# Optimization experiments

Measured on AMD Instinct MI355X. Metric: run time of the kernel, lower is better.

## Reference

```python
import jax, jax.numpy as jnp
import numpy as np

H = 8            # kv heads
R = 2            # qhead_ratio -> hq = 16 query heads
D = 128          # head_size
DEG = 2          # power degree
GATE_OFFSET = 6.906768  # ~log(999), gates start near 1


def setup_inputs() -> dict:
    key = jax.random.key(0)
    ks = jax.random.split(key, 7)
    B, T, C = 1, 2048, 2048
    q_dim = H * R * D   # 2048
    kv_dim = H * D      # 1024
    s = 0.02
    return {
        "hidden_states": jax.random.normal(ks[0], (B, T, C), dtype=jnp.float32),
        "Wq": jax.random.normal(ks[1], (C, q_dim), dtype=jnp.float32) * s,
        "Wk": jax.random.normal(ks[2], (C, kv_dim), dtype=jnp.float32) * s,
        "Wv": jax.random.normal(ks[3], (C, kv_dim), dtype=jnp.float32) * s,
        "Wg": jax.random.normal(ks[4], (C, H), dtype=jnp.float32) * s,
        "Wc": jax.random.normal(ks[5], (q_dim, C), dtype=jnp.float32) * s,
        "bc": jnp.zeros((C,), dtype=jnp.float32),
    }


def _power_attention(q, k, v, log_g):
    # q: [B,T,hq,D], k/v: [B,T,H,D], log_g: [B,T,H]
    B, T, hq, d = q.shape
    scale = 1.0 / d ** 0.5
    # GQA: query head i uses kv head i // R (q was viewed as (B,T,H,R,D))
    k = jnp.repeat(k, R, axis=2)            # [B,T,hq,D]
    v = jnp.repeat(v, R, axis=2)            # [B,T,hq,D]
    logG = jnp.cumsum(log_g, axis=1)        # [B,T,H]
    logG = jnp.repeat(logG, R, axis=2)      # [B,T,hq]
    logG = jnp.transpose(logG, (0, 2, 1))   # [B,hq,T]
    qk = jnp.einsum('bthd,bshd->bhts', q, k) * scale   # [B,hq,T,T]
    a = qk ** DEG                                       # even degree -> >= 0
    # gating decay exp(logG_t - logG_s) <= 1 for s <= t
    gate = logG[:, :, :, None] - logG[:, :, None, :]    # [B,hq,T,T]
    causal = jnp.tril(jnp.ones((T, T), dtype=bool))
    a = jnp.where(causal, a * jnp.exp(gate), 0.0)
    norm = jnp.sum(a, axis=-1) + 1e-6                   # [B,hq,T]
    y = jnp.einsum('bhts,bshd->bthd', a, v)             # [B,T,hq,D]
    y = y / jnp.transpose(norm, (0, 2, 1))[..., None]
    return y


def reference(hidden_states, Wq, Wk, Wv, Wg, Wc, bc):
    B, T, C = hidden_states.shape
    q = (hidden_states @ Wq).reshape(B, T, H * R, D)
    k = (hidden_states @ Wk).reshape(B, T, H, D)
    v = (hidden_states @ Wv).reshape(B, T, H, D)
    g = hidden_states @ Wg                              # [B,T,H]
    log_g = jax.nn.log_sigmoid(GATE_OFFSET + g.astype(jnp.float32))
    y = _power_attention(q, k, v, log_g)                # [B,T,hq,D]
    y = y.reshape(B, T, H * R * D)
    return y @ Wc + bc
```

## Files before the change

### kernel.cpp

```cpp
#include <hip/hip_runtime.h>

typedef unsigned short u16;
typedef unsigned int u32;
typedef unsigned long long u64;
typedef __bf16 bf16x8 __attribute__((ext_vector_type(8)));
typedef float f32x4 __attribute__((ext_vector_type(4)));

union FragAB {
  bf16x8 v;
  u16 u[8];
  u32 w[4];
  u64 d2[2];
};

__device__ __forceinline__ u16 f2bf(float f) {
  u32 u = __builtin_bit_cast(u32, f);
  u += 0x7fffu + ((u >> 16) & 1u);
  return (u16)(u >> 16);
}

__device__ __forceinline__ void gload_lds16(const void* g, void* l) {
  __builtin_amdgcn_global_load_lds((__attribute__((address_space(1))) void*)g,
                                   (__attribute__((address_space(3))) void*)l, 16, 0, 0);
}

__device__ __forceinline__ int permcol(int n) {
  int k = n & 31;
  return (n & ~31) | ((k & 12) << 1) | ((k & 16) >> 2) | (k & 3);
}

__global__ __launch_bounds__(256) void conv_bf16_kernel(const float* __restrict__ in,
                                                        u16* __restrict__ out, int n4) {
  int i = blockIdx.x * 256 + threadIdx.x;
  if (i >= n4) return;
  float4 v = ((const float4*)in)[i];
  u32 lo = (u32)f2bf(v.x) | ((u32)f2bf(v.y) << 16);
  u32 hi = (u32)f2bf(v.z) | ((u32)f2bf(v.w) << 16);
  ((u32*)out)[2 * i] = lo;
  ((u32*)out)[2 * i + 1] = hi;
}

__global__ __launch_bounds__(256) void tconv_kernel(const float* __restrict__ in,
                                                    u16* __restrict__ out, int K, int N) {
  __shared__ float tile[32][33];
  int col = threadIdx.x & 31;
  int row0 = threadIdx.x >> 5;
  int kb = blockIdx.y * 32, nb = blockIdx.x * 32;
#pragma unroll
  for (int i = 0; i < 4; i++) {
    int r = row0 + i * 8;
    tile[r][col] = in[(size_t)(kb + r) * N + nb + col];
  }
  __syncthreads();
#pragma unroll
  for (int i = 0; i < 4; i++) {
    int r = row0 + i * 8;
    out[(size_t)(nb + r) * K + kb + col] = f2bf(tile[col][r]);
  }
}

__global__ __launch_bounds__(256) void tconv3_kernel(const float* __restrict__ Wq,
                                                     const float* __restrict__ Wk,
                                                     const float* __restrict__ Wv,
                                                     u16* __restrict__ slab) {
  __shared__ float tile[32][33];
  const int z = blockIdx.z;
  const float* src = (z < 2) ? Wq : (z == 2 ? Wk : Wv);
  const int srcN = (z < 2) ? 2048 : 1024;
  const int colBase = (z == 1) ? 1024 : 0;
  const int dstRowBase = z * 1024;
  int col = threadIdx.x & 31;
  int row0 = threadIdx.x >> 5;
  int kb = blockIdx.y * 32, nb = blockIdx.x * 32;
#pragma unroll
  for (int i = 0; i < 4; i++) {
    int r = row0 + i * 8;
    tile[r][col] = src[(size_t)(kb + r) * srcN + colBase + nb + col];
  }
  __syncthreads();
#pragma unroll
  for (int i = 0; i < 4; i++) {
    int r = row0 + i * 8;
    slab[(size_t)(dstRowBase + nb + r) * 2048 + kb + col] = f2bf(tile[col][r]);
  }
}

__global__ __launch_bounds__(256) void gate_kernel(const float* __restrict__ hs,
                                                   const float* __restrict__ Wg,
                                                   float* __restrict__ lgt) {
  int lane = threadIdx.x & 63, wid = threadIdx.x >> 6;
  int t = blockIdx.x * 4 + wid;
  float acc[8] = {0.f, 0.f, 0.f, 0.f, 0.f, 0.f, 0.f, 0.f};
  for (int c = lane; c < 2048; c += 64) {
    float x = hs[(size_t)t * 2048 + c];
    float4 w0 = *(const float4*)&Wg[c * 8];
    float4 w1 = *(const float4*)&Wg[c * 8 + 4];
    acc[0] += x * w0.x; acc[1] += x * w0.y; acc[2] += x * w0.z; acc[3] += x * w0.w;
    acc[4] += x * w1.x; acc[5] += x * w1.y; acc[6] += x * w1.z; acc[7] += x * w1.w;
  }
#pragma unroll
  for (int h = 0; h < 8; h++) {
    float v = acc[h];
    for (int m = 1; m < 64; m <<= 1) v += __shfl_xor(v, m, 64);
    if (lane == 0) {
      float x = 6.906768f + v;
      lgt[h * 2048 + t] = -log1pf(__expf(-x));
    }
  }
}

__global__ __launch_bounds__(256) void cumsum_kernel(const float* __restrict__ lgt,
                                                     float* __restrict__ logG) {
  int h = blockIdx.x;
  __shared__ float buf[2048];
  for (int i = threadIdx.x; i < 2048; i += 256) buf[i] = lgt[h * 2048 + i];
  __syncthreads();
  for (int off = 1; off < 2048; off <<= 1) {
    float tmp[8];
#pragma unroll
    for (int j = 0; j < 8; j++) {
      int i = threadIdx.x + j * 256;
      tmp[j] = (i >= off) ? buf[i - off] : 0.f;
    }
    __syncthreads();
#pragma unroll
    for (int j = 0; j < 8; j++) {
      int i = threadIdx.x + j * 256;
      buf[i] += tmp[j];
    }
    __syncthreads();
  }
  for (int i = threadIdx.x; i < 2048; i += 256) logG[h * 2048 + i] = buf[i];
}

template <int MODE, int NT>
__global__ __launch_bounds__(512) void gemm_bf16(const u16* __restrict__ A,
                                                 const u16* __restrict__ BT,
                                                 void* __restrict__ C0,
                                                 void* __restrict__ C1,
                                                 int permLim) {
  __shared__ __align__(16) u16 As[128 * 64];
  __shared__ __align__(16) u16 Bs[128 * 64];
  constexpr int nwg = 16 * NT * (MODE == 2 ? 2 : 1);
  constexpr int cpx = nwg >> 3;
  const int raw = (int)blockIdx.x;
  const int wg = (raw & 7) * cpx + (raw >> 3);
  int bx, by, z;
  if constexpr (MODE == 2) {
    z = wg & 1;
    int t = wg >> 1;
    by = t >> 4;
    bx = t & 15;
  } else {
    z = 0;
    by = wg >> 4;
    bx = wg & 15;
  }
  const int kBeg = (MODE == 2) ? z * 1024 : 0;
  const int kEnd = (MODE == 2) ? kBeg + 1024 : 2048;
  constexpr int N = NT * 128;

  const int tid = threadIdx.x;
  const int lane = tid & 63, wid = tid >> 6;
  const int m0 = bx * 128, n0 = by * 128;
  const int wr = wid >> 2, wc = wid & 3;
  const int l15 = lane & 15, kg = lane >> 4;

  f32x4 acc[4][2];
#pragma unroll
  for (int i = 0; i < 4; i++)
#pragma unroll
    for (int j = 0; j < 2; j++) acc[i][j] = f32x4{0.f, 0.f, 0.f, 0.f};

  const int ch0 = (wid * 2) * 64 + lane;
  const int ch1 = ch0 + 64;
  const int r0 = ch0 >> 3, u0 = (ch0 & 7) ^ (r0 & 7);
  const int r1 = ch1 >> 3, u1 = (ch1 & 7) ^ (r1 & 7);
  const u16* Asrc0 = A + (size_t)(m0 + r0) * 2048 + u0 * 8;
  const u16* Asrc1 = A + (size_t)(m0 + r1) * 2048 + u1 * 8;
  const u16* Bsrc0 = BT + (size_t)(n0 + r0) * 2048 + u0 * 8;
  const u16* Bsrc1 = BT + (size_t)(n0 + r1) * 2048 + u1 * 8;
  u16* Adst0 = As + (wid * 2) * 512;
  u16* Bdst0 = Bs + (wid * 2) * 512;

  for (int k0 = kBeg; k0 < kEnd; k0 += 64) {
    __syncthreads();
    gload_lds16(Asrc0 + k0, Adst0);
    gload_lds16(Asrc1 + k0, Adst0 + 512);
    gload_lds16(Bsrc0 + k0, Bdst0);
    gload_lds16(Bsrc1 + k0, Bdst0 + 512);
    __syncthreads();

#pragma unroll
    for (int ks = 0; ks < 2; ks++) {
      FragAB af[4], bfr[2];
      const int ul = ks * 4 + (kg >> 1);
#pragma unroll
      for (int mt = 0; mt < 4; mt++) {
        int row = wr * 64 + mt * 16 + l15;
        int sw = row & 7;
        const u16* p = &As[row * 64 + (kg & 1) * 4];
        af[mt].d2[0] = *(const u64*)&p[(ul ^ sw) << 3];
        af[mt].d2[1] = *(const u64*)&p[((ul + 2) ^ sw) << 3];
      }
#pragma unroll
      for (int nt = 0; nt < 2; nt++) {
        int row = wc * 32 + nt * 16 + l15;
        int sw = row & 7;
        const u16* p = &Bs[row * 64 + (kg & 1) * 4];
        bfr[nt].d2[0] = *(const u64*)&p[(ul ^ sw) << 3];
        bfr[nt].d2[1] = *(const u64*)&p[((ul + 2) ^ sw) << 3];
      }
#pragma unroll
      for (int mt = 0; mt < 4; mt++)
#pragma unroll
        for (int nt = 0; nt < 2; nt++)
          acc[mt][nt] = __builtin_amdgcn_mfma_f32_16x16x32_bf16(af[mt].v, bfr[nt].v, acc[mt][nt], 0, 0, 0);
    }
  }

#pragma unroll
  for (int mt = 0; mt < 4; mt++) {
#pragma unroll
    for (int re = 0; re < 4; re++) {
      int m = m0 + wr * 64 + mt * 16 + kg * 4 + re;
#pragma unroll
      for (int nt = 0; nt < 2; nt++) {
        int n = n0 + wc * 32 + nt * 16 + l15;
        float v = acc[mt][nt][re];
        if constexpr (MODE == 2) {
          float* P = z ? (float*)C1 : (float*)C0;
          P[(size_t)m * N + n] = v;
        } else {
          int nw = (n < permLim) ? permcol(n) : n;
          ((u16*)C0)[(size_t)m * N + nw] = f2bf(v);
        }
      }
    }
  }
}

__global__ __launch_bounds__(256, 2) void power_attn(const u16* __restrict__ QKV,
                                                     const float* __restrict__ logG,
                                                     float* __restrict__ y0p,
                                                     float* __restrict__ y1p,
                                                     float* __restrict__ npart) {
  __shared__ __align__(16) u16 Ks[2 * 64 * 128];
  __shared__ __align__(16) u16 Vt[2 * 128 * 64];
  __shared__ float eS[2 * 64];

  const int raw = (int)blockIdx.x;
  const int orig = (raw & 7) * 64 + (raw >> 3);
  const int hq = orig >> 5;
  const int j_ = orig & 31;
  const int half = j_ & 1;
  const int bslot = j_ >> 1;
  const int qa = (bslot + (hq >> 1) * 3) & 15;
  const int qt = (hq & 1) ? (15 - qa) : qa;
  const int hk = hq >> 1;
  const int t0 = qt * 128;

  const int tid = threadIdx.x, lane = tid & 63, wid = tid >> 6;
  const int l15 = lane & 15, kg = lane >> 4;
  const int l7 = l15 & 7;

  const int s4 = tid & 15, dgrp = tid >> 4;
  const int ubase = 4 * (s4 >> 3) + (s4 & 3);
  const int vhb = (s4 >> 2) & 1;

  const u16* Kbase = QKV + 2048 + hk * 128;
  const u16* Vbase = QKV + 3072 + hk * 128 + dgrp * 8;
  const float* lgh = logG + hk * 2048;

  FragAB qf[2][4];
  float celg[2];
  int myT[2];
  const float scale2 = 0.0078125f;
#pragma unroll
  for (int cg = 0; cg < 2; cg++) {
    myT[cg] = t0 + wid * 16 + cg * 64 + l15;
    const u16* qrow = QKV + (size_t)myT[cg] * 4096 + hq * 128;
#pragma unroll
    for (int ks = 0; ks < 4; ks++) qf[cg][ks].v = *(const bf16x8*)(qrow + ks * 32 + kg * 8);
    celg[cg] = scale2 * __expf(lgh[myT[cg]]);
  }

  f32x4 yacc[8][2];
#pragma unroll
  for (int i = 0; i < 8; i++)
#pragma unroll
    for (int c = 0; c < 2; c++) yacc[i][c] = f32x4{0.f, 0.f, 0.f, 0.f};
  float nacc[2] = {0.f, 0.f};

  const int itBeg = half ? (qt + 1) : 0;
  const int itEnd = half ? (2 * qt + 2) : (qt + 1);

  auto stageK = [&](int s0, int bb) {
#pragma unroll
    for (int c = 0; c < 4; c++) {
      int ch = (wid * 4 + c) * 64 + lane;
      int row = ch >> 4, du = ch & 15;
      int su = du ^ (row & 7);
      gload_lds16(Kbase + (size_t)(s0 + row) * 4096 + su * 8, &Ks[bb * 8192 + (wid * 4 + c) * 512]);
    }
  };
  auto loadV = [&](int s0, uint4* vr) {
#pragma unroll
    for (int r = 0; r < 4; r++) vr[r] = *(const uint4*)(Vbase + (size_t)(s0 + 4 * s4 + r) * 4096);
  };
  auto writeV = [&](int bb, const uint4* vr) {
    u16* vd = &Vt[bb * 8192];
    const u32* w0 = (const u32*)&vr[0];
    const u32* w1 = (const u32*)&vr[1];
    const u32* w2 = (const u32*)&vr[2];
    const u32* w3 = (const u32*)&vr[3];
#pragma unroll
    for (int i = 0; i < 8; i++) {
      u32 sel = (i & 1) ? 0x07060302u : 0x05040100u;
      u32 lo = __builtin_amdgcn_perm(w1[i >> 1], w0[i >> 1], sel);
      u32 hi = __builtin_amdgcn_perm(w3[i >> 1], w2[i >> 1], sel);
      int d = dgrp * 8 + i;
      int e = d * 64 + 8 * (ubase ^ i) + 4 * vhb;
      *(u64*)&vd[e] = (u64)lo | ((u64)hi << 32);
    }
  };

  {
    uint4 vr[4];
    stageK(itBeg * 64, 0);
    loadV(itBeg * 64, vr);
    float ee = (tid < 64) ? lgh[itBeg * 64 + tid] : 0.f;
    writeV(0, vr);
    if (tid < 64) eS[tid] = __expf(-ee);
  }
  __syncthreads();

  for (int it = itBeg; it < itEnd; it++) {
    const int cur = (it - itBeg) & 1;
    const int s0 = it * 64;
    const bool hasNext = (it + 1 < itEnd);
    uint4 vr[4];
    float ee = 0.f;
    if (hasNext) {
      stageK(s0 + 64, cur ^ 1);
      loadV(s0 + 64, vr);
      if (tid < 64) ee = lgh[s0 + 64 + tid];
    }

    const u16* kb = &Ks[cur * 8192];
    f32x4 sacc[4][2];
#pragma unroll
    for (int mt = 0; mt < 4; mt++)
#pragma unroll
      for (int cg = 0; cg < 2; cg++) sacc[mt][cg] = f32x4{0.f, 0.f, 0.f, 0.f};
    __builtin_amdgcn_s_setprio(1);
#pragma unroll
    for (int ks = 0; ks < 4; ks++) {
#pragma unroll
      for (int mt = 0; mt < 4; mt++) {
        FragAB af;
        af.v = *(const bf16x8*)&kb[(mt * 16 + l15) * 128 + 8 * ((4 * ks + kg) ^ l7)];
        sacc[mt][0] = __builtin_amdgcn_mfma_f32_16x16x32_bf16(af.v, qf[0][ks].v, sacc[mt][0], 0, 0, 0);
        sacc[mt][1] = __builtin_amdgcn_mfma_f32_16x16x32_bf16(af.v, qf[1][ks].v, sacc[mt][1], 0, 0, 0);
      }
    }
    __builtin_amdgcn_s_setprio(0);

    FragAB pa[2][2];
    const bool need_mask = (it >= 2 * qt);
#pragma unroll
    for (int mt = 0; mt < 4; mt++) {
      f32x4 ev = *(const f32x4*)&eS[cur * 64 + mt * 16 + kg * 4];
#pragma unroll
      for (int cg = 0; cg < 2; cg++) {
        u32 pb[4];
#pragma unroll
        for (int r = 0; r < 4; r++) {
          float x = sacc[mt][cg][r];
          float p = x * x * celg[cg] * ev[r];
          if (need_mask) {
            int s = s0 + mt * 16 + kg * 4 + r;
            p = (s <= myT[cg]) ? p : 0.f;
          }
          nacc[cg] += p;
          pb[r] = __builtin_bit_cast(u32, p) + 0x8000u;
        }
        pa[cg][mt >> 1].w[(mt & 1) * 2 + 0] = __builtin_amdgcn_perm(pb[1], pb[0], 0x07060302u);
        pa[cg][mt >> 1].w[(mt & 1) * 2 + 1] = __builtin_amdgcn_perm(pb[3], pb[2], 0x07060302u);
      }
    }

    const u16* vb = &Vt[cur * 8192];
    const int x0 = 8 * (kg ^ l7);
    __builtin_amdgcn_s_setprio(1);
#pragma unroll
    for (int ksv = 0; ksv < 2; ksv++) {
      const int xo = x0 ^ (ksv * 32);
#pragma unroll
      for (int nt = 0; nt < 8; nt++) {
        FragAB bfv;
        bfv.v = *(const bf16x8*)&vb[(nt * 16 + l15) * 64 + xo];
        yacc[nt][0] = __builtin_amdgcn_mfma_f32_16x16x32_bf16(pa[0][ksv].v, bfv.v, yacc[nt][0], 0, 0, 0);
        yacc[nt][1] = __builtin_amdgcn_mfma_f32_16x16x32_bf16(pa[1][ksv].v, bfv.v, yacc[nt][1], 0, 0, 0);
      }
    }
    __builtin_amdgcn_s_setprio(0);

    if (hasNext) {
      writeV(cur ^ 1, vr);
      if (tid < 64) eS[(cur ^ 1) * 64 + tid] = __expf(-ee);
    }
    __syncthreads();
  }

  float* yp = half ? y1p : y0p;
  float* np = npart + half * (16 * 2048);
#pragma unroll
  for (int cg = 0; cg < 2; cg++) {
    float nf = nacc[cg];
    nf += __shfl_xor(nf, 16, 64);
    nf += __shfl_xor(nf, 32, 64);
    if (lane < 16) np[hq * 2048 + t0 + wid * 16 + cg * 64 + lane] = nf;
#pragma unroll
    for (int re = 0; re < 4; re++) {
      int trow = t0 + wid * 16 + cg * 64 + kg * 4 + re;
      float* yrow = yp + (size_t)trow * 2048 + hq * 128;
#pragma unroll
      for (int nt = 0; nt < 8; nt++) yrow[nt * 16 + l15] = yacc[nt][cg][re];
    }
  }
}

__global__ __launch_bounds__(256) void combine_kernel(const float* __restrict__ y0,
                                                      const float* __restrict__ y1,
                                                      const float* __restrict__ npart,
                                                      u16* __restrict__ yb) {
  int i = blockIdx.x * 256 + threadIdx.x;
  int e0 = i << 2;
  int t = e0 >> 11;
  int hq = (e0 >> 7) & 15;
  float nn = npart[hq * 2048 + t] + npart[32768 + hq * 2048 + t] + 1e-6f;
  float inv = 1.0f / nn;
  float4 a = ((const float4*)y0)[i];
  float4 b = ((const float4*)y1)[i];
  u32 lo = (u32)f2bf((a.x + b.x) * inv) | ((u32)f2bf((a.y + b.y) * inv) << 16);
  u32 hi = (u32)f2bf((a.z + b.z) * inv) | ((u32)f2bf((a.w + b.w) * inv) << 16);
  ((u32*)yb)[2 * i] = lo;
  ((u32*)yb)[2 * i + 1] = hi;
}

__global__ __launch_bounds__(256) void combine2_kernel(const float* __restrict__ p0,
                                                       float* __restrict__ out,
                                                       const float* __restrict__ bias) {
  int i = blockIdx.x * 256 + threadIdx.x;
  int col = (i << 2) & 2047;
  float4 a = ((const float4*)p0)[i];
  float4 b = ((const float4*)out)[i];
  float4 bb = *(const float4*)&bias[col];
  float4 r;
  r.x = a.x + b.x + bb.x;
  r.y = a.y + b.y + bb.y;
  r.z = a.z + b.z + bb.z;
  r.w = a.w + b.w + bb.w;
  ((float4*)out)[i] = r;
}

extern "C" void kernel_launch(void* const* d_in, const int* in_sizes, int n_in,
                              void* d_out, int out_size, void* d_ws, size_t ws_size,
                              hipStream_t stream) {
  (void)in_sizes; (void)n_in; (void)out_size; (void)ws_size;
  const float* hs = (const float*)d_in[0];
  const float* Wq = (const float*)d_in[1];
  const float* Wk = (const float*)d_in[2];
  const float* Wv = (const float*)d_in[3];
  const float* Wg = (const float*)d_in[4];
  const float* Wc = (const float*)d_in[5];
  const float* bc = (const float*)d_in[6];
  float* out = (float*)d_out;

  char* ws = (char*)d_ws;
  const size_t MB = 1024 * 1024;
  u16* slab   = (u16*)(ws);
  u16* hs_bf  = (u16*)(ws + 16 * MB);
  u16* qkv_bf = (u16*)(ws + 24 * MB);
  float* y0p  = (float*)(ws + 40 * MB);
  float* npart = (float*)(ws + 56 * MB);
  float* lgt  = (float*)(ws + 56 * MB + 262144);
  float* logG = (float*)(ws + 56 * MB + 327680);
  float* y1p = out;
  u16* y_bf = hs_bf;
  u16* WcT = slab;

  conv_bf16_kernel<<<4096, 256, 0, stream>>>(hs, hs_bf, 2048 * 2048 / 4);
  tconv3_kernel<<<dim3(32, 64, 4), 256, 0, stream>>>(Wq, Wk, Wv, slab);

  gemm_bf16<1, 32><<<512, 512, 0, stream>>>(hs_bf, slab, qkv_bf, nullptr, 3072);

  gate_kernel<<<512, 256, 0, stream>>>(hs, Wg, lgt);
  cumsum_kernel<<<8, 256, 0, stream>>>(lgt, logG);

  tconv_kernel<<<dim3(64, 64), 256, 0, stream>>>(Wc, WcT, 2048, 2048);

  power_attn<<<dim3(512), 256, 0, stream>>>(qkv_bf, logG, y0p, y1p, npart);
  combine_kernel<<<4096, 256, 0, stream>>>(y0p, y1p, npart, y_bf);

  gemm_bf16<2, 16><<<512, 512, 0, stream>>>(y_bf, WcT, y0p, out, 0);
  combine2_kernel<<<4096, 256, 0, stream>>>(y0p, out, bc);
}
```

Before: 199.2 us.

## Double-buffer GEMM LDS tiles and pre-permute K columns for single 128-bit fragment loads

The GEMM now uses two LDS buffers and issues the global-to-LDS loads for the next K tile before computing the current one. This removes one barrier per iteration and lets memory latency overlap with MFMA work. The producers (hs conversion, weight transposes, combine) now write K columns in a permuted order, so each lane can read its MFMA fragment with one 16-byte LDS load instead of two 8-byte loads. The cost is double the LDS footprint, which may lower occupancy, and correctness depends on both GEMM operands using the same K permutation.

```diff
diff --git a/kernel.cpp b/kernel.cpp
--- a/kernel.cpp
+++ b/kernel.cpp
@@ -29,15 +29,18 @@
   return (n & ~31) | ((k & 12) << 1) | ((k & 16) >> 2) | (k & 3);
 }
 
-__global__ __launch_bounds__(256) void conv_bf16_kernel(const float* __restrict__ in,
+__global__ __launch_bounds__(256) void conv_perm_kernel(const float* __restrict__ in,
                                                         u16* __restrict__ out, int n4) {
   int i = blockIdx.x * 256 + threadIdx.x;
   if (i >= n4) return;
   float4 v = ((const float4*)in)[i];
-  u32 lo = (u32)f2bf(v.x) | ((u32)f2bf(v.y) << 16);
-  u32 hi = (u32)f2bf(v.z) | ((u32)f2bf(v.w) << 16);
-  ((u32*)out)[2 * i] = lo;
-  ((u32*)out)[2 * i + 1] = hi;
+  u64 pk = (u64)f2bf(v.x) | ((u64)f2bf(v.y) << 16) | ((u64)f2bf(v.z) << 32) |
+           ((u64)f2bf(v.w) << 48);
+  int col = (i << 2) & 2047;
+  int g = (col >> 2) & 7;
+  int ncol = (col & ~31) | ((2 * (g & 3) + (g >> 2)) << 2);
+  size_t row = (size_t)(i >> 9);
+  *(u64*)&out[row * 2048 + ncol] = pk;
 }
 
 __global__ __launch_bounds__(256) void tconv_kernel(const float* __restrict__ in,
@@ -46,6 +49,7 @@
   int col = threadIdx.x & 31;
   int row0 = threadIdx.x >> 5;
   int kb = blockIdx.y * 32, nb = blockIdx.x * 32;
+  int pcol = permcol(col);
 #pragma unroll
   for (int i = 0; i < 4; i++) {
     int r = row0 + i * 8;
@@ -55,7 +59,7 @@
 #pragma unroll
   for (int i = 0; i < 4; i++) {
     int r = row0 + i * 8;
-    out[(size_t)(nb + r) * K + kb + col] = f2bf(tile[col][r]);
+    out[(size_t)(nb + r) * K + kb + pcol] = f2bf(tile[col][r]);
   }
 }
 
@@ -72,6 +76,7 @@
   int col = threadIdx.x & 31;
   int row0 = threadIdx.x >> 5;
   int kb = blockIdx.y * 32, nb = blockIdx.x * 32;
+  int pcol = permcol(col);
 #pragma unroll
   for (int i = 0; i < 4; i++) {
     int r = row0 + i * 8;
@@ -81,7 +86,7 @@
 #pragma unroll
   for (int i = 0; i < 4; i++) {
     int r = row0 + i * 8;
-    slab[(size_t)(dstRowBase + nb + r) * 2048 + kb + col] = f2bf(tile[col][r]);
+    slab[(size_t)(dstRowBase + nb + r) * 2048 + kb + pcol] = f2bf(tile[col][r]);
   }
 }
 
@@ -134,13 +139,13 @@
 }
 
 template <int MODE, int NT>
-__global__ __launch_bounds__(512) void gemm_bf16(const u16* __restrict__ A,
-                                                 const u16* __restrict__ BT,
-                                                 void* __restrict__ C0,
-                                                 void* __restrict__ C1,
-                                                 int permLim) {
-  __shared__ __align__(16) u16 As[128 * 64];
-  __shared__ __align__(16) u16 Bs[128 * 64];
+__global__ __launch_bounds__(512, 4) void gemm_v2(const u16* __restrict__ A,
+                                                  const u16* __restrict__ BT,
+                                                  void* __restrict__ C0,
+                                                  void* __restrict__ C1,
+                                                  int permLim) {
+  __shared__ __align__(16) u16 As[2 * 128 * 64];
+  __shared__ __align__(16) u16 Bs[2 * 128 * 64];
   constexpr int nwg = 16 * NT * (MODE == 2 ? 2 : 1);
   constexpr int cpx = nwg >> 3;
   const int raw = (int)blockIdx.x;
@@ -172,44 +177,44 @@
 #pragma unroll
     for (int j = 0; j < 2; j++) acc[i][j] = f32x4{0.f, 0.f, 0.f, 0.f};
 
-  const int ch0 = (wid * 2) * 64 + lane;
-  const int ch1 = ch0 + 64;
-  const int r0 = ch0 >> 3, u0 = (ch0 & 7) ^ (r0 & 7);
-  const int r1 = ch1 >> 3, u1 = (ch1 & 7) ^ (r1 & 7);
-  const u16* Asrc0 = A + (size_t)(m0 + r0) * 2048 + u0 * 8;
-  const u16* Asrc1 = A + (size_t)(m0 + r1) * 2048 + u1 * 8;
-  const u16* Bsrc0 = BT + (size_t)(n0 + r0) * 2048 + u0 * 8;
-  const u16* Bsrc1 = BT + (size_t)(n0 + r1) * 2048 + u1 * 8;
-  u16* Adst0 = As + (wid * 2) * 512;
-  u16* Bdst0 = Bs + (wid * 2) * 512;
-
+  const int c0 = (wid * 2) * 64 + lane;
+  const int c1 = c0 + 64;
+  const int r0 = c0 >> 3, s0u = (c0 & 7) ^ (r0 & 7);
+  const int r1 = c1 >> 3, s1u = (c1 & 7) ^ (r1 & 7);
+  const u16* Asrc0 = A + (size_t)(m0 + r0) * 2048 + s0u * 8;
+  const u16* Asrc1 = A + (size_t)(m0 + r1) * 2048 + s1u * 8;
+  const u16* Bsrc0 = BT + (size_t)(n0 + r0) * 2048 + s0u * 8;
+  const u16* Bsrc1 = BT + (size_t)(n0 + r1) * 2048 + s1u * 8;
+
+  auto stage = [&](int buf, int k0) {
+    u16* Ad = As + buf * 8192 + (wid * 2) * 512;
+    u16* Bd = Bs + buf * 8192 + (wid * 2) * 512;
+    gload_lds16(Asrc0 + k0, Ad);
+    gload_lds16(Asrc1 + k0, Ad + 512);
+    gload_lds16(Bsrc0 + k0, Bd);
+    gload_lds16(Bsrc1 + k0, Bd + 512);
+  };
+
+  stage(0, kBeg);
+  __syncthreads();
+
+  int cur = 0;
   for (int k0 = kBeg; k0 < kEnd; k0 += 64) {
-    __syncthreads();
-    gload_lds16(Asrc0 + k0, Adst0);
-    gload_lds16(Asrc1 + k0, Adst0 + 512);
-    gload_lds16(Bsrc0 + k0, Bdst0);
-    gload_lds16(Bsrc1 + k0, Bdst0 + 512);
-    __syncthreads();
-
+    if (k0 + 64 < kEnd) stage(cur ^ 1, k0 + 64);
+    const u16* Ab = As + cur * 8192;
+    const u16* Bb = Bs + cur * 8192;
 #pragma unroll
     for (int ks = 0; ks < 2; ks++) {
       FragAB af[4], bfr[2];
-      const int ul = ks * 4 + (kg >> 1);
 #pragma unroll
       for (int mt = 0; mt < 4; mt++) {
         int row = wr * 64 + mt * 16 + l15;
-        int sw = row & 7;
-        const u16* p = &As[row * 64 + (kg & 1) * 4];
-        af[mt].d2[0] = *(const u64*)&p[(ul ^ sw) << 3];
-        af[mt].d2[1] = *(const u64*)&p[((ul + 2) ^ sw) << 3];
+        af[mt].v = *(const bf16x8*)&Ab[row * 64 + 8 * ((ks * 4 + kg) ^ (row & 7))];
       }
 #pragma unroll
       for (int nt = 0; nt < 2; nt++) {
         int row = wc * 32 + nt * 16 + l15;
-        int sw = row & 7;
-        const u16* p = &Bs[row * 64 + (kg & 1) * 4];
-        bfr[nt].d2[0] = *(const u64*)&p[(ul ^ sw) << 3];
-        bfr[nt].d2[1] = *(const u64*)&p[((ul + 2) ^ sw) << 3];
+        bfr[nt].v = *(const bf16x8*)&Bb[row * 64 + 8 * ((ks * 4 + kg) ^ (row & 7))];
       }
 #pragma unroll
       for (int mt = 0; mt < 4; mt++)
@@ -217,6 +222,8 @@
         for (int nt = 0; nt < 2; nt++)
           acc[mt][nt] = __builtin_amdgcn_mfma_f32_16x16x32_bf16(af[mt].v, bfr[nt].v, acc[mt][nt], 0, 0, 0);
     }
+    __syncthreads();
+    cur ^= 1;
   }
 
 #pragma unroll
@@ -443,10 +450,12 @@
   float inv = 1.0f / nn;
   float4 a = ((const float4*)y0)[i];
   float4 b = ((const float4*)y1)[i];
-  u32 lo = (u32)f2bf((a.x + b.x) * inv) | ((u32)f2bf((a.y + b.y) * inv) << 16);
-  u32 hi = (u32)f2bf((a.z + b.z) * inv) | ((u32)f2bf((a.w + b.w) * inv) << 16);
-  ((u32*)yb)[2 * i] = lo;
-  ((u32*)yb)[2 * i + 1] = hi;
+  u64 pk = (u64)f2bf((a.x + b.x) * inv) | ((u64)f2bf((a.y + b.y) * inv) << 16) |
+           ((u64)f2bf((a.z + b.z) * inv) << 32) | ((u64)f2bf((a.w + b.w) * inv) << 48);
+  int col = e0 & 2047;
+  int g = (col >> 2) & 7;
+  int ncol = (col & ~31) | ((2 * (g & 3) + (g >> 2)) << 2);
+  *(u64*)&yb[(size_t)t * 2048 + ncol] = pk;
 }
 
 __global__ __launch_bounds__(256) void combine2_kernel(const float* __restrict__ p0,
@@ -491,10 +500,10 @@
   u16* y_bf = hs_bf;
   u16* WcT = slab;
 
-  conv_bf16_kernel<<<4096, 256, 0, stream>>>(hs, hs_bf, 2048 * 2048 / 4);
+  conv_perm_kernel<<<4096, 256, 0, stream>>>(hs, hs_bf, 2048 * 2048 / 4);
   tconv3_kernel<<<dim3(32, 64, 4), 256, 0, stream>>>(Wq, Wk, Wv, slab);
 
-  gemm_bf16<1, 32><<<512, 512, 0, stream>>>(hs_bf, slab, qkv_bf, nullptr, 3072);
+  gemm_v2<1, 32><<<512, 512, 0, stream>>>(hs_bf, slab, qkv_bf, nullptr, 3072);
 
   gate_kernel<<<512, 256, 0, stream>>>(hs, Wg, lgt);
   cumsum_kernel<<<8, 256, 0, stream>>>(lgt, logG);
@@ -504,6 +513,6 @@
   power_attn<<<dim3(512), 256, 0, stream>>>(qkv_bf, logG, y0p, y1p, npart);
   combine_kernel<<<4096, 256, 0, stream>>>(y0p, y1p, npart, y_bf);
 
-  gemm_bf16<2, 16><<<512, 512, 0, stream>>>(y_bf, WcT, y0p, out, 0);
+  gemm_v2<2, 16><<<512, 512, 0, stream>>>(y_bf, WcT, y0p, out, 0);
   combine2_kernel<<<4096, 256, 0, stream>>>(y0p, out, bc);
 }
```

Result: faster. 164.2 us (-17.6%).
